# Kernel tuning notes

Measured on AMD Instinct MI355X. Metric: run time of the kernel, lower is better.

The kernel has to match this reference:

```python
import jax, jax.numpy as jnp
from jax import lax
import numpy as np
import math


def make_kernel():
    # StyleGAN2 blur kernel [1,3,3,1], normalized outer product
    k = jnp.array([1.0, 3.0, 3.0, 1.0], dtype=jnp.float32)
    k2 = jnp.outer(k, k)
    return k2 / jnp.sum(k2)


def upfirdn2d(x, kernel, up=1, pad=(0, 0)):
    # x: [B,C,H,W]; depthwise FIR filter, optional zero-insert upsampling
    C = x.shape[1]
    w = jnp.tile(jnp.flip(kernel)[None, None].astype(x.dtype), (C, 1, 1, 1))
    # torch upfirdn pads up-1 trailing zeros after the last sample; lhs_dilation
    # only inserts zeros between samples, so fold the extra zeros into pad[1].
    p = (pad[0], pad[1] + up - 1)
    return lax.conv_general_dilated(
        x, w, (1, 1), (p, p), lhs_dilation=(up, up), feature_group_count=C)


def modulated_conv(x, weight, style, demodulate=True, up=False):
    # per-sample weight modulation + demodulation, executed as grouped conv
    B, Cin, H, W = x.shape
    Cout, _, k, _ = weight.shape
    scale = 1.0 / math.sqrt(Cin * k * k)
    w = scale * weight[None] * style[:, None, :, None, None]  # [B,Cout,Cin,k,k]
    if demodulate:
        d = lax.rsqrt(jnp.sum(w * w, axis=(2, 3, 4)) + 1e-8)
        w = w * d[:, :, None, None, None]
    xg = x.reshape(1, B * Cin, H, W)
    if up:
        # conv_transpose2d(stride=2, pad=0) == lhs-dilated conv with flipped kernel
        wg = jnp.flip(w, (-2, -1)).reshape(B * Cout, Cin, k, k)
        out = lax.conv_general_dilated(
            xg, wg, (1, 1), ((k - 1, k - 1), (k - 1, k - 1)),
            lhs_dilation=(2, 2), feature_group_count=B)
    else:
        pad = k // 2
        out = lax.conv_general_dilated(
            xg, w.reshape(B * Cout, Cin, k, k), (1, 1),
            ((pad, pad), (pad, pad)), feature_group_count=B)
    return out.reshape(B, Cout, out.shape[2], out.shape[3])


def fused_lrelu(x, bias):
    y = x + bias[None, :, None, None]
    return jnp.where(y >= 0, y, 0.2 * y) * math.sqrt(2.0)


def setup_inputs() -> dict:
    key = jax.random.key(0)
    ks = jax.random.split(key, 12)
    B, C, H = 8, 512, 32
    f = jnp.float32
    return {
        "x": jax.random.normal(ks[0], (B, C, H, H), f),
        "skip": jax.random.normal(ks[1], (B, 3, H, H), f),
        "w1": jax.random.normal(ks[2], (C, C, 3, 3), f),
        "b1": jnp.zeros((C,), f),
        "s1": jax.random.normal(ks[3], (B, C), f),
        "nw1": jax.random.normal(ks[4], (1,), f) * 0.1,
        "n1": jax.random.normal(ks[5], (B, 1, 2 * H, 2 * H), f),
        "w2": jax.random.normal(ks[6], (C, C, 3, 3), f),
        "b2": jnp.zeros((C,), f),
        "s2": jax.random.normal(ks[7], (B, C), f),
        "nw2": jax.random.normal(ks[8], (1,), f) * 0.1,
        "n2": jax.random.normal(ks[9], (B, 1, 2 * H, 2 * H), f),
        "w_rgb": jax.random.normal(ks[10], (3, C, 1, 1), f),
        "b_rgb": jnp.zeros((3,), f),
        "s_rgb": jax.random.normal(ks[11], (B, C), f),
    }


def reference(x, skip, w1, b1, s1, nw1, n1, w2, b2, s2, nw2, n2,
              w_rgb, b_rgb, s_rgb):
    kern = make_kernel()
    # conv1: upsampling modulated conv + blur (Blur with upsample_factor=2)
    out = modulated_conv(x, w1, s1, demodulate=True, up=True)
    out = upfirdn2d(out, kern * 4.0, up=1, pad=(1, 1))
    out = out + nw1 * n1          # NoiseInjection
    out = fused_lrelu(out, b1)    # FusedLeakyReLU
    # conv2: plain modulated conv
    out = modulated_conv(out, w2, s2, demodulate=True)
    out = out + nw2 * n2
    out = fused_lrelu(out, b2)
    # ToRGB: 1x1 mod conv, no demodulation, + bias; skip = rgb + upsample(skip)
    rgb = modulated_conv(out, w_rgb, s_rgb, demodulate=False)
    rgb = rgb + b_rgb[None, :, None, None]
    skip_up = upfirdn2d(skip, kern * 4.0, up=2, pad=(2, 1))
    return rgb + skip_up
```

## Files before the change

kernel.cpp:

```cpp
#include <hip/hip_runtime.h>
#include <stdint.h>

typedef unsigned short ushort_t;
typedef unsigned int uint_t;
typedef __bf16 bf16x8 __attribute__((ext_vector_type(8)));
typedef float f32x4 __attribute__((ext_vector_type(4)));

#define GLOBAL_AS __attribute__((address_space(1)))
#define LDS_AS    __attribute__((address_space(3)))

#define SCALE_CONV 0.014731391f
#define SCALE_RGB  0.044194174f
#define SQRT2_F    1.41421356237f

__device__ __forceinline__ void async_cp16(const void* g, void* l) {
  __builtin_amdgcn_global_load_lds((const GLOBAL_AS uint_t*)g,
                                   (LDS_AS uint_t*)l, 16, 0, 0);
}
__device__ __forceinline__ ushort_t f2bf(float v) {
  union { float f; uint_t u; } c; c.f = v;
  uint_t r = c.u + 0x7fffu + ((c.u >> 16) & 1u);
  return (ushort_t)(r >> 16);
}
__device__ __forceinline__ float bf2f(ushort_t u) {
  union { uint_t u; float f; } c; c.u = ((uint_t)u) << 16;
  return c.f;
}

__global__ __launch_bounds__(256) void prep_x1(
    const float* __restrict__ x, const float* __restrict__ s1,
    ushort_t* __restrict__ xpad) {
  __shared__ ushort_t t[32 * 520];
  const int b  = blockIdx.x >> 5;
  const int j1 = blockIdx.x & 31;
  for (int idx = threadIdx.x; idx < 512 * 32; idx += 256) {
    int ci = idx >> 5, j2 = idx & 31;
    float v = x[(size_t)(b * 512 + ci) * 1024 + j1 * 32 + j2];
    v *= s1[b * 512 + ci] * SCALE_CONV;
    t[j2 * 520 + ci] = f2bf(v);
  }
  __syncthreads();
  for (int idx = threadIdx.x; idx < 32 * 512; idx += 256) {
    int j2 = idx >> 9, ci = idx & 511;
    xpad[((size_t)(b * 34 + j1 + 1) * 34 + (j2 + 1)) * 512 + ci] = t[j2 * 520 + ci];
  }
}

__global__ __launch_bounds__(256) void prep_w(
    const float* __restrict__ w, ushort_t* __restrict__ wt) {
  int t = blockIdx.x * 256 + threadIdx.x;
  int ci = t & 511, co = t >> 9;
  const float* wp = w + (size_t)(co * 512 + ci) * 9;
#pragma unroll
  for (int u = 0; u < 9; ++u)
    wt[((size_t)u * 512 + co) * 512 + ci] = f2bf(wp[u]);
}

__global__ __launch_bounds__(256) void demod_k(
    const float* __restrict__ w1, const float* __restrict__ s1, float* __restrict__ d1,
    const float* __restrict__ w2, const float* __restrict__ s2, float* __restrict__ d2) {
  const int co = blockIdx.x, b = blockIdx.y;
  const float* w = blockIdx.z ? w2 : w1;
  const float* s = blockIdx.z ? s2 : s1;
  float*       d = blockIdx.z ? d2 : d1;
  float acc = 0.f;
  for (int ci = threadIdx.x; ci < 512; ci += 256) {
    const float* wp = w + (size_t)(co * 512 + ci) * 9;
    float ws = 0.f;
#pragma unroll
    for (int u = 0; u < 9; ++u) ws += wp[u] * wp[u];
    float sv = s[b * 512 + ci];
    acc += ws * sv * sv;
  }
#pragma unroll
  for (int o = 32; o; o >>= 1) acc += __shfl_xor(acc, o);
  __shared__ float red[4];
  if ((threadIdx.x & 63) == 0) red[threadIdx.x >> 6] = acc;
  __syncthreads();
  if (threadIdx.x == 0) {
    float tot = red[0] + red[1] + red[2] + red[3];
    d[b * 512 + co] = rsqrtf(tot * (1.f / 4608.f) + 1e-8f);
  }
}

__constant__ int           c_ph_off[4]  = {0, 4, 6, 8};
__constant__ int           c_ph_ntap[4] = {4, 2, 2, 1};
__constant__ unsigned char c_tap_u1[9]  = {0,0,1,1, 0,1, 1,1, 1};
__constant__ unsigned char c_tap_u2[9]  = {0,1,0,1, 1,1, 0,1, 1};
__constant__ unsigned char c_tap_pl[9]  = {8,6,2,0, 7,1, 5,3, 4};

template <int MODE>
__global__ __launch_bounds__(256, 4) void gemm_conv(
    const ushort_t* __restrict__ inp, const ushort_t* __restrict__ wt,
    const float* __restrict__ dmod, const float* __restrict__ noise,
    const float* __restrict__ nw, const float* __restrict__ bias,
    const float* __restrict__ snext, float snext_scale,
    ushort_t* __restrict__ outp) {
  __shared__ ushort_t ldsA[128 * 32];
  __shared__ ushort_t ldsB[128 * 32];

  const int tid  = threadIdx.x;
  const int lane = tid & 63;
  const int wv   = tid >> 6;
  const int wm   = wv & 1;
  const int wn   = wv >> 1;
  const int l16  = lane & 15;
  const int quad = lane >> 4;

  const int mtile = blockIdx.x;
  const int ntile = blockIdx.y;
  const int a  = (MODE == 0) ? blockIdx.z : 0;
  const int a1 = a >> 1, a2 = a & 1;

  const int qg = ((lane & 3) - (lane >> 3)) & 3;
  const char* pA[2];
  const char* pB[2];
#pragma unroll
  for (int t = 0; t < 2; ++t) {
    int row = wv * 32 + t * 16 + (lane >> 2);
    int m   = mtile * 128 + row;
    size_t pix;
    if (MODE == 0) {
      if (m > 8711) m = 8711;
      int b = m / 1089, rr = m % 1089;
      int p1 = rr / 33, p2 = rr % 33;
      pix = ((size_t)(b * 34 + p1) * 34 + p2) * 512;
    } else {
      int b = m >> 12, o1 = (m >> 6) & 63, o2 = m & 63;
      pix = ((size_t)(b * 66 + o1 + 1) * 66 + (o2 + 1)) * 512;
    }
    pA[t] = (const char*)inp + pix * 2 + qg * 16;
    int n = ntile * 128 + row;
    pB[t] = (const char*)wt + (size_t)n * 1024 + qg * 16;
  }
  char* ldsAdst[2];
  char* ldsBdst[2];
#pragma unroll
  for (int t = 0; t < 2; ++t) {
    ldsAdst[t] = (char*)ldsA + (wv * 128 + t * 64) * 16;
    ldsBdst[t] = (char*)ldsB + (wv * 128 + t * 64) * 16;
  }

  int offA[4], offB[4];
#pragma unroll
  for (int i = 0; i < 4; ++i) {
    int r  = wm * 64 + i * 16 + l16;
    int rn = wn * 64 + i * 16 + l16;
    offA[i] = r  * 32 + (((quad + (r  >> 1)) & 3) << 3);
    offB[i] = rn * 32 + (((quad + (rn >> 1)) & 3) << 3);
  }

  f32x4 acc[4][4];
#pragma unroll
  for (int i = 0; i < 4; ++i)
#pragma unroll
    for (int j = 0; j < 4; ++j) acc[i][j] = (f32x4){0.f, 0.f, 0.f, 0.f};

  const int ntap = (MODE == 0) ? c_ph_ntap[a] : 9;
#pragma unroll 1
  for (int ti = 0; ti < ntap; ++ti) {
    int aoff, boff;
    if (MODE == 0) {
      int e = c_ph_off[a] + ti;
      aoff = ((int)c_tap_u1[e] * 34 + (int)c_tap_u2[e]) * 1024;
      boff = (int)c_tap_pl[e] * 524288;
    } else {
      aoff = ((ti / 3 - 1) * 66 + (ti % 3 - 1)) * 1024;
      boff = ti * 524288;
    }
#pragma unroll 1
    for (int kc = 0; kc < 16; ++kc) {
      const int koff = kc * 64;
      __syncthreads();
      async_cp16(pA[0] + aoff + koff, ldsAdst[0]);
      async_cp16(pA[1] + aoff + koff, ldsAdst[1]);
      async_cp16(pB[0] + boff + koff, ldsBdst[0]);
      async_cp16(pB[1] + boff + koff, ldsBdst[1]);
      __syncthreads();
      bf16x8 af[4], bg[4];
#pragma unroll
      for (int i = 0; i < 4; ++i) af[i] = *reinterpret_cast<const bf16x8*>(ldsA + offA[i]);
#pragma unroll
      for (int j = 0; j < 4; ++j) bg[j] = *reinterpret_cast<const bf16x8*>(ldsB + offB[j]);
#pragma unroll
      for (int i = 0; i < 4; ++i)
#pragma unroll
        for (int j = 0; j < 4; ++j)
          acc[i][j] = __builtin_amdgcn_mfma_f32_16x16x32_bf16(af[i], bg[j], acc[i][j], 0, 0, 0);
    }
  }

  int co_[4];
#pragma unroll
  for (int j = 0; j < 4; ++j) co_[j] = ntile * 128 + wn * 64 + j * 16 + l16;

  if (MODE == 0) {
#pragma unroll
    for (int i = 0; i < 4; ++i) {
#pragma unroll
      for (int r = 0; r < 4; ++r) {
        int m = mtile * 128 + wm * 64 + i * 16 + quad * 4 + r;
        if (m < 8712) {
          int b = m / 1089, rr = m % 1089;
          int p1 = rr / 33, p2 = rr % 33;
          if ((a1 == 0 || p1 < 32) && (a2 == 0 || p2 < 32)) {
            int o1 = 2 * p1 + a1, o2 = 2 * p2 + a2;
            size_t ob = ((size_t)(b * 67 + o1 + 1) * 67 + (o2 + 1)) * 512;
#pragma unroll
            for (int j = 0; j < 4; ++j)
              outp[ob + co_[j]] = f2bf(acc[i][j][r] * dmod[b * 512 + co_[j]]);
          }
        }
      }
    }
  } else {
    const int b = mtile >> 5;
    const float nwv = nw[0];
    float dj_[4], sj_[4], bj_[4];
#pragma unroll
    for (int j = 0; j < 4; ++j) {
      dj_[j] = dmod[b * 512 + co_[j]];
      sj_[j] = snext[b * 512 + co_[j]] * snext_scale;
      bj_[j] = bias[co_[j]];
    }
#pragma unroll
    for (int i = 0; i < 4; ++i) {
#pragma unroll
      for (int r = 0; r < 4; ++r) {
        int m = mtile * 128 + wm * 64 + i * 16 + quad * 4 + r;
        int o1 = (m >> 6) & 63, o2 = m & 63;
        float nz = nwv * noise[(b << 12) + (o1 << 6) + o2];
        size_t ob = ((size_t)(b * 64 + o1) * 64 + o2) * 512;
#pragma unroll
        for (int j = 0; j < 4; ++j) {
          float v = acc[i][j][r] * dj_[j] + nz + bj_[j];
          v = (v >= 0.f ? v : 0.2f * v) * SQRT2_F;
          v *= sj_[j];
          outp[ob + co_[j]] = f2bf(v);
        }
      }
    }
  }
}

__global__ __launch_bounds__(256) void blur_noise_act(
    const ushort_t* __restrict__ y1pad, const float* __restrict__ noise,
    const float* __restrict__ nw, const float* __restrict__ bias,
    const float* __restrict__ s2, ushort_t* __restrict__ out1pad) {
  const int cg  = threadIdx.x & 63;
  const int pg  = blockIdx.x * 4 + (threadIdx.x >> 6);
  const int b   = pg >> 10;
  const int q1  = (pg >> 4) & 63;
  const int q2g = (pg & 15) * 4;
  const float cw[4] = {0.25f, 0.75f, 0.75f, 0.25f};

  float acc[4][8];
#pragma unroll
  for (int j = 0; j < 4; ++j)
#pragma unroll
    for (int e = 0; e < 8; ++e) acc[j][e] = 0.f;

#pragma unroll
  for (int t2 = 0; t2 < 7; ++t2) {
    int cc = q2g + t2;
    float vt[8];
#pragma unroll
    for (int e = 0; e < 8; ++e) vt[e] = 0.f;
#pragma unroll
    for (int t1 = 0; t1 < 4; ++t1) {
      const ushort_t* p = y1pad + ((size_t)(b * 67 + q1 + t1) * 67 + cc) * 512 + cg * 8;
      ushort_t v[8];
      *(uint4*)v = *(const uint4*)p;
#pragma unroll
      for (int e = 0; e < 8; ++e) vt[e] += cw[t1] * bf2f(v[e]);
    }
#pragma unroll
    for (int j = 0; j < 4; ++j) {
      int t = t2 - j;
      if (t >= 0 && t < 4) {
#pragma unroll
        for (int e = 0; e < 8; ++e) acc[j][e] += cw[t] * vt[e];
      }
    }
  }

  const float nwv = nw[0];
  float bj[8], sj[8];
#pragma unroll
  for (int e = 0; e < 8; ++e) {
    bj[e] = bias[cg * 8 + e];
    sj[e] = s2[b * 512 + cg * 8 + e] * SCALE_CONV;
  }
#pragma unroll
  for (int j = 0; j < 4; ++j) {
    int q2 = q2g + j;
    float nz = nwv * noise[(b << 12) + (q1 << 6) + q2];
    ushort_t o[8];
#pragma unroll
    for (int e = 0; e < 8; ++e) {
      float v = acc[j][e] + nz + bj[e];
      v = (v >= 0.f ? v : 0.2f * v) * SQRT2_F * sj[e];
      o[e] = f2bf(v);
    }
    *(uint4*)(out1pad + ((size_t)(b * 66 + q1 + 1) * 66 + (q2 + 1)) * 512 + cg * 8) = *(uint4*)o;
  }
}

__global__ __launch_bounds__(256) void torgb_skip(
    const ushort_t* __restrict__ out2s, const float* __restrict__ wrgb,
    const float* __restrict__ brgb, const float* __restrict__ skip,
    float* __restrict__ out) {
  const int lane = threadIdx.x & 63;
  const int pix  = blockIdx.x * 4 + (threadIdx.x >> 6);
  const int b = pix >> 12, o1 = (pix >> 6) & 63, o2 = pix & 63;
  const ushort_t* src = out2s + (size_t)pix * 512 + lane * 8;
  ushort_t v[8];
  *(uint4*)v = *(const uint4*)src;
  float s0 = 0.f, s1 = 0.f, s2 = 0.f;
#pragma unroll
  for (int e = 0; e < 8; ++e) {
    float xv = bf2f(v[e]);
    int ci = lane * 8 + e;
    s0 += xv * wrgb[ci];
    s1 += xv * wrgb[512 + ci];
    s2 += xv * wrgb[1024 + ci];
  }
#pragma unroll
  for (int o = 32; o; o >>= 1) {
    s0 += __shfl_xor(s0, o);
    s1 += __shfl_xor(s1, o);
    s2 += __shfl_xor(s2, o);
  }
  if (lane < 3) {
    float v3 = (lane == 0) ? s0 : (lane == 1 ? s1 : s2);
    int P1 = o1 >> 1, P2 = o2 >> 1;
    int jy0, jy1, jx0, jx1;
    float wy0, wy1, wx0, wx1;
    if ((o1 & 1) == 0) { jy0 = P1 - 1; wy0 = .25f; jy1 = P1;     wy1 = .75f; }
    else               { jy0 = P1;     wy0 = .75f; jy1 = P1 + 1; wy1 = .25f; }
    if ((o2 & 1) == 0) { jx0 = P2 - 1; wx0 = .25f; jx1 = P2;     wx1 = .75f; }
    else               { jx0 = P2;     wx0 = .75f; jx1 = P2 + 1; wx1 = .25f; }
    const float* sp = skip + (size_t)(b * 3 + lane) * 1024;
    float sv = 0.f;
    if (jy0 >= 0 && jy0 < 32) {
      if (jx0 >= 0 && jx0 < 32) sv += wy0 * wx0 * sp[jy0 * 32 + jx0];
      if (jx1 >= 0 && jx1 < 32) sv += wy0 * wx1 * sp[jy0 * 32 + jx1];
    }
    if (jy1 >= 0 && jy1 < 32) {
      if (jx0 >= 0 && jx0 < 32) sv += wy1 * wx0 * sp[jy1 * 32 + jx0];
      if (jx1 >= 0 && jx1 < 32) sv += wy1 * wx1 * sp[jy1 * 32 + jx1];
    }
    out[((size_t)(b * 3 + lane) << 12) + (o1 << 6) + o2] = v3 + brgb[lane] + sv;
  }
}

extern "C" void kernel_launch(void* const* d_in, const int* in_sizes, int n_in,
                              void* d_out, int out_size, void* d_ws, size_t ws_size,
                              hipStream_t stream) {
  const float* x    = (const float*)d_in[0];
  const float* skip = (const float*)d_in[1];
  const float* w1   = (const float*)d_in[2];
  const float* b1   = (const float*)d_in[3];
  const float* s1   = (const float*)d_in[4];
  const float* nw1  = (const float*)d_in[5];
  const float* n1   = (const float*)d_in[6];
  const float* w2   = (const float*)d_in[7];
  const float* b2   = (const float*)d_in[8];
  const float* s2   = (const float*)d_in[9];
  const float* nw2  = (const float*)d_in[10];
  const float* n2   = (const float*)d_in[11];
  const float* wrgb = (const float*)d_in[12];
  const float* brgb = (const float*)d_in[13];
  const float* srgb = (const float*)d_in[14];

  char* ws = (char*)d_ws;
  const size_t XPAD_B  = (size_t)8 * 34 * 34 * 512 * 2;
  const size_t Y1PAD_B = (size_t)8 * 67 * 67 * 512 * 2;
  const size_t OUT1_B  = (size_t)8 * 66 * 66 * 512 * 2;
  const size_t WT_B    = (size_t)9 * 512 * 512 * 2;
  size_t off = 0;
  ushort_t* xpad1   = (ushort_t*)(ws + off); off += XPAD_B;
  ushort_t* y1pad   = (ushort_t*)(ws + off); off += Y1PAD_B;
  ushort_t* out1pad = (ushort_t*)(ws + off); off += OUT1_B;
  ushort_t* wt1     = (ushort_t*)(ws + off); off += WT_B;
  ushort_t* wt2     = (ushort_t*)(ws + off); off += WT_B;
  float*    d1      = (float*)(ws + off);    off += 8 * 512 * 4;
  float*    d2      = (float*)(ws + off);    off += 8 * 512 * 4;
  ushort_t* out2s   = y1pad;

  hipMemsetAsync(xpad1, 0, XPAD_B, stream);
  hipMemsetAsync(y1pad, 0, Y1PAD_B, stream);
  hipMemsetAsync(out1pad, 0, OUT1_B, stream);

  prep_x1<<<256, 256, 0, stream>>>(x, s1, xpad1);
  prep_w<<<1024, 256, 0, stream>>>(w1, wt1);
  prep_w<<<1024, 256, 0, stream>>>(w2, wt2);
  demod_k<<<dim3(512, 8, 2), 256, 0, stream>>>(w1, s1, d1, w2, s2, d2);

  gemm_conv<0><<<dim3(69, 4, 4), 256, 0, stream>>>(
      xpad1, wt1, d1, nullptr, nullptr, nullptr, nullptr, 0.f, y1pad);
  blur_noise_act<<<2048, 256, 0, stream>>>(y1pad, n1, nw1, b1, s2, out1pad);
  gemm_conv<1><<<dim3(256, 4, 1), 256, 0, stream>>>(
      out1pad, wt2, d2, n2, nw2, b2, srgb, SCALE_RGB, out2s);
  torgb_skip<<<8192, 256, 0, stream>>>(out2s, wrgb, brgb, skip, (float*)d_out);
}
```

Baseline: 406.1 us.

## Double GEMM K-chunk, fold demod sums into weight prep, zero only borders

The conv GEMM now stages 64-wide K chunks in LDS with an 8-way XOR swizzle, halving barrier count per tap. Occupancy is lowered to 3 blocks per CU. Weight square sums are computed during bf16 weight prep and reduced by a small transposed demod kernel, and the two prep_w launches are merged. Full-buffer memsets are replaced by a kernel that zeroes only padding borders, relying on the GEMMs to write every interior pixel and reusing y1pad as scratch.

```diff
diff --git a/kernel.cpp b/kernel.cpp
--- a/kernel.cpp
+++ b/kernel.cpp
@@ -47,40 +47,60 @@
 }
 
 __global__ __launch_bounds__(256) void prep_w(
-    const float* __restrict__ w, ushort_t* __restrict__ wt) {
+    const float* __restrict__ w1, const float* __restrict__ w2,
+    ushort_t* __restrict__ wt1, ushort_t* __restrict__ wt2,
+    float* __restrict__ wsqT1, float* __restrict__ wsqT2) {
   int t = blockIdx.x * 256 + threadIdx.x;
-  int ci = t & 511, co = t >> 9;
+  const float* w  = (t < 262144) ? w1 : w2;
+  ushort_t*   wt  = (t < 262144) ? wt1 : wt2;
+  float*      wq  = (t < 262144) ? wsqT1 : wsqT2;
+  int tt = t & 262143;
+  int ci = tt & 511, co = tt >> 9;
   const float* wp = w + (size_t)(co * 512 + ci) * 9;
-#pragma unroll
-  for (int u = 0; u < 9; ++u)
-    wt[((size_t)u * 512 + co) * 512 + ci] = f2bf(wp[u]);
-}
-
-__global__ __launch_bounds__(256) void demod_k(
-    const float* __restrict__ w1, const float* __restrict__ s1, float* __restrict__ d1,
-    const float* __restrict__ w2, const float* __restrict__ s2, float* __restrict__ d2) {
-  const int co = blockIdx.x, b = blockIdx.y;
-  const float* w = blockIdx.z ? w2 : w1;
-  const float* s = blockIdx.z ? s2 : s1;
-  float*       d = blockIdx.z ? d2 : d1;
-  float acc = 0.f;
-  for (int ci = threadIdx.x; ci < 512; ci += 256) {
-    const float* wp = w + (size_t)(co * 512 + ci) * 9;
-    float ws = 0.f;
-#pragma unroll
-    for (int u = 0; u < 9; ++u) ws += wp[u] * wp[u];
-    float sv = s[b * 512 + ci];
-    acc += ws * sv * sv;
-  }
-#pragma unroll
-  for (int o = 32; o; o >>= 1) acc += __shfl_xor(acc, o);
-  __shared__ float red[4];
-  if ((threadIdx.x & 63) == 0) red[threadIdx.x >> 6] = acc;
+  float sq = 0.f;
+#pragma unroll
+  for (int u = 0; u < 9; ++u) {
+    float v = wp[u];
+    sq += v * v;
+    wt[((size_t)u * 512 + co) * 512 + ci] = f2bf(v);
+  }
+  wq[ci * 512 + co] = sq;
+}
+
+__global__ __launch_bounds__(512) void demod2(
+    const float* __restrict__ wsqT1, const float* __restrict__ s1, float* __restrict__ d1,
+    const float* __restrict__ wsqT2, const float* __restrict__ s2, float* __restrict__ d2) {
+  const float* wq = blockIdx.y ? wsqT2 : wsqT1;
+  const float* s  = blockIdx.y ? s2 : s1;
+  float*       d  = blockIdx.y ? d2 : d1;
+  const int b  = blockIdx.x;
+  const int co = threadIdx.x;
+  __shared__ float ssq[512];
+  float sv = s[b * 512 + co];
+  ssq[co] = sv * sv;
   __syncthreads();
-  if (threadIdx.x == 0) {
-    float tot = red[0] + red[1] + red[2] + red[3];
-    d[b * 512 + co] = rsqrtf(tot * (1.f / 4608.f) + 1e-8f);
-  }
+  float a = 0.f;
+#pragma unroll 4
+  for (int ci = 0; ci < 512; ++ci) a += wq[ci * 512 + co] * ssq[ci];
+  d[b * 512 + co] = rsqrtf(a * (1.f / 4608.f) + 1e-8f);
+}
+
+__global__ __launch_bounds__(256) void border_zero(
+    ushort_t* __restrict__ xpad, ushort_t* __restrict__ ypad, ushort_t* __restrict__ opad) {
+  const int z = blockIdx.z;
+  ushort_t* p = (z == 0) ? xpad : (z == 1 ? ypad : opad);
+  const int W = (z == 0) ? 34 : (z == 1 ? 67 : 66);
+  const int nb = 4 * W - 4;
+  const int t = blockIdx.x * 256 + threadIdx.x;
+  const int pix = t >> 6, ch = (t & 63) * 8;
+  if (pix >= nb) return;
+  const int b = blockIdx.y;
+  int y, x;
+  if (pix < W)          { y = 0;     x = pix; }
+  else if (pix < 2 * W) { y = W - 1; x = pix - W; }
+  else { int q = pix - 2 * W; y = 1 + (q >> 1); x = (q & 1) ? W - 1 : 0; }
+  uint4 z4 = {0, 0, 0, 0};
+  *(uint4*)(p + ((size_t)(b * W + y) * W + x) * 512 + ch) = z4;
 }
 
 __constant__ int           c_ph_off[4]  = {0, 4, 6, 8};
@@ -90,14 +110,14 @@
 __constant__ unsigned char c_tap_pl[9]  = {8,6,2,0, 7,1, 5,3, 4};
 
 template <int MODE>
-__global__ __launch_bounds__(256, 4) void gemm_conv(
+__global__ __launch_bounds__(256, 3) void gemm_conv(
     const ushort_t* __restrict__ inp, const ushort_t* __restrict__ wt,
     const float* __restrict__ dmod, const float* __restrict__ noise,
     const float* __restrict__ nw, const float* __restrict__ bias,
     const float* __restrict__ snext, float snext_scale,
     ushort_t* __restrict__ outp) {
-  __shared__ ushort_t ldsA[128 * 32];
-  __shared__ ushort_t ldsB[128 * 32];
+  __shared__ ushort_t ldsA[128 * 64];
+  __shared__ ushort_t ldsB[128 * 64];
 
   const int tid  = threadIdx.x;
   const int lane = tid & 63;
@@ -112,12 +132,12 @@
   const int a  = (MODE == 0) ? blockIdx.z : 0;
   const int a1 = a >> 1, a2 = a & 1;
 
-  const int qg = ((lane & 3) - (lane >> 3)) & 3;
-  const char* pA[2];
-  const char* pB[2];
-#pragma unroll
-  for (int t = 0; t < 2; ++t) {
-    int row = wv * 32 + t * 16 + (lane >> 2);
+  const int cl = ((lane & 7) - (lane >> 3)) & 7;
+  const char* pA[4];
+  const char* pB[4];
+#pragma unroll
+  for (int t = 0; t < 4; ++t) {
+    int row = wv * 32 + t * 8 + (lane >> 3);
     int m   = mtile * 128 + row;
     size_t pix;
     if (MODE == 0) {
@@ -129,16 +149,16 @@
       int b = m >> 12, o1 = (m >> 6) & 63, o2 = m & 63;
       pix = ((size_t)(b * 66 + o1 + 1) * 66 + (o2 + 1)) * 512;
     }
-    pA[t] = (const char*)inp + pix * 2 + qg * 16;
+    pA[t] = (const char*)inp + pix * 2 + cl * 16;
     int n = ntile * 128 + row;
-    pB[t] = (const char*)wt + (size_t)n * 1024 + qg * 16;
-  }
-  char* ldsAdst[2];
-  char* ldsBdst[2];
-#pragma unroll
-  for (int t = 0; t < 2; ++t) {
-    ldsAdst[t] = (char*)ldsA + (wv * 128 + t * 64) * 16;
-    ldsBdst[t] = (char*)ldsB + (wv * 128 + t * 64) * 16;
+    pB[t] = (const char*)wt + (size_t)n * 1024 + cl * 16;
+  }
+  char* dstA[4];
+  char* dstB[4];
+#pragma unroll
+  for (int t = 0; t < 4; ++t) {
+    dstA[t] = (char*)ldsA + wv * 4096 + t * 1024;
+    dstB[t] = (char*)ldsB + wv * 4096 + t * 1024;
   }
 
   int offA[4], offB[4];
@@ -146,8 +166,8 @@
   for (int i = 0; i < 4; ++i) {
     int r  = wm * 64 + i * 16 + l16;
     int rn = wn * 64 + i * 16 + l16;
-    offA[i] = r  * 32 + (((quad + (r  >> 1)) & 3) << 3);
-    offB[i] = rn * 32 + (((quad + (rn >> 1)) & 3) << 3);
+    offA[i] = r  * 64 + (((quad + r)  & 7) << 3);
+    offB[i] = rn * 64 + (((quad + rn) & 7) << 3);
   }
 
   f32x4 acc[4][4];
@@ -169,24 +189,28 @@
       boff = ti * 524288;
     }
 #pragma unroll 1
-    for (int kc = 0; kc < 16; ++kc) {
-      const int koff = kc * 64;
+    for (int kc = 0; kc < 8; ++kc) {
+      const int koff = kc * 128;
       __syncthreads();
-      async_cp16(pA[0] + aoff + koff, ldsAdst[0]);
-      async_cp16(pA[1] + aoff + koff, ldsAdst[1]);
-      async_cp16(pB[0] + boff + koff, ldsBdst[0]);
-      async_cp16(pB[1] + boff + koff, ldsBdst[1]);
+#pragma unroll
+      for (int t = 0; t < 4; ++t) async_cp16(pA[t] + aoff + koff, dstA[t]);
+#pragma unroll
+      for (int t = 0; t < 4; ++t) async_cp16(pB[t] + boff + koff, dstB[t]);
       __syncthreads();
-      bf16x8 af[4], bg[4];
-#pragma unroll
-      for (int i = 0; i < 4; ++i) af[i] = *reinterpret_cast<const bf16x8*>(ldsA + offA[i]);
-#pragma unroll
-      for (int j = 0; j < 4; ++j) bg[j] = *reinterpret_cast<const bf16x8*>(ldsB + offB[j]);
-#pragma unroll
-      for (int i = 0; i < 4; ++i)
-#pragma unroll
-        for (int j = 0; j < 4; ++j)
-          acc[i][j] = __builtin_amdgcn_mfma_f32_16x16x32_bf16(af[i], bg[j], acc[i][j], 0, 0, 0);
+#pragma unroll
+      for (int kk = 0; kk < 2; ++kk) {
+        const int kx = kk << 5;
+        bf16x8 af[4], bg[4];
+#pragma unroll
+        for (int i = 0; i < 4; ++i) af[i] = *reinterpret_cast<const bf16x8*>(ldsA + (offA[i] ^ kx));
+#pragma unroll
+        for (int j = 0; j < 4; ++j) bg[j] = *reinterpret_cast<const bf16x8*>(ldsB + (offB[j] ^ kx));
+#pragma unroll
+        for (int i = 0; i < 4; ++i)
+#pragma unroll
+          for (int j = 0; j < 4; ++j)
+            acc[i][j] = __builtin_amdgcn_mfma_f32_16x16x32_bf16(af[i], bg[j], acc[i][j], 0, 0, 0);
+      }
     }
   }
 
@@ -386,16 +410,14 @@
   ushort_t* wt2     = (ushort_t*)(ws + off); off += WT_B;
   float*    d1      = (float*)(ws + off);    off += 8 * 512 * 4;
   float*    d2      = (float*)(ws + off);    off += 8 * 512 * 4;
-  ushort_t* out2s   = y1pad;
-
-  hipMemsetAsync(xpad1, 0, XPAD_B, stream);
-  hipMemsetAsync(y1pad, 0, Y1PAD_B, stream);
-  hipMemsetAsync(out1pad, 0, OUT1_B, stream);
+  ushort_t* out2s  = y1pad;
+  float*    wsqT1  = (float*)y1pad;
+  float*    wsqT2  = wsqT1 + 512 * 512;
 
   prep_x1<<<256, 256, 0, stream>>>(x, s1, xpad1);
-  prep_w<<<1024, 256, 0, stream>>>(w1, wt1);
-  prep_w<<<1024, 256, 0, stream>>>(w2, wt2);
-  demod_k<<<dim3(512, 8, 2), 256, 0, stream>>>(w1, s1, d1, w2, s2, d2);
+  prep_w<<<2048, 256, 0, stream>>>(w1, w2, wt1, wt2, wsqT1, wsqT2);
+  demod2<<<dim3(8, 2), 512, 0, stream>>>(wsqT1, s1, d1, wsqT2, s2, d2);
+  border_zero<<<dim3(66, 8, 3), 256, 0, stream>>>(xpad1, y1pad, out1pad);
 
   gemm_conv<0><<<dim3(69, 4, 4), 256, 0, stream>>>(
       xpad1, wt1, d1, nullptr, nullptr, nullptr, nullptr, 0.f, y1pad);
```

After: 393.8 us. -3.0%, faster.
